# Kernel optimization log

Hardware: AMD Instinct MI355X
Metric: run time of the kernel (lower is better)

The kernel has to match this reference:

```python
import jax, jax.numpy as jnp
import numpy as np

B, N, M, D = 4, 4096, 4096, 128


def setup_inputs() -> dict:
    key = jax.random.key(0)
    kk, kq, kv = jax.random.split(key, 3)
    return {
        "k": jax.random.normal(kk, (B, N, D), dtype=jnp.float32),
        "q": jax.random.normal(kq, (B, M, D), dtype=jnp.float32),
        "v": jax.random.normal(kv, (B, M, D), dtype=jnp.float32),
    }


def reference(k, q, v):
    # scores: [B, N, M] = k @ q^T
    scores = jnp.einsum("bnd,bmd->bnm", k, q)
    # Original uses nn.Softmax() with no dim; torch's legacy rule resolves
    # dim=0 for 3-D inputs, so softmax is over the batch axis, applied twice.
    w = jax.nn.softmax(jax.nn.softmax(scores, axis=0), axis=0)
    out = jnp.einsum("bnm,bmd->bnd", w, v)
    return out
```

## Files before the change

### kernel.cpp

```cpp
#include <hip/hip_runtime.h>
#include <hip/hip_bf16.h>

#define NB 4
#define NN 4096
#define MM 4096
#define DD 128
#define BN 32
#define BM 64
#define NCH 4
#define OUT_ELEMS ((size_t)NB * NN * DD)

using f32x4  = __attribute__((ext_vector_type(4))) float;
using bf16x8 = __attribute__((ext_vector_type(8))) short;

__device__ __forceinline__ float fast_exp2(float x) {
  return __builtin_amdgcn_exp2f(x);
}

__device__ __forceinline__ int rfl(int x) {
  return __builtin_amdgcn_readfirstlane(x);
}

__device__ __forceinline__ short f2bf(float x) {
  union { __hip_bfloat16 h; short s; } u;
  u.h = __float2bfloat16(x);
  return u.s;
}

__device__ __forceinline__ bf16x8 pack8(const float* __restrict__ p) {
  float4 a = *(const float4*)p;
  float4 b = *(const float4*)(p + 4);
  bf16x8 r;
  r[0] = f2bf(a.x); r[1] = f2bf(a.y); r[2] = f2bf(a.z); r[3] = f2bf(a.w);
  r[4] = f2bf(b.x); r[5] = f2bf(b.y); r[6] = f2bf(b.z); r[7] = f2bf(b.w);
  return r;
}

__global__ __launch_bounds__(256) void zero_out_kernel(float4* __restrict__ out) {
  out[(size_t)blockIdx.x * 256 + threadIdx.x] = (float4){0.f, 0.f, 0.f, 0.f};
}

__global__ __launch_bounds__(256) void cvt_frag_kernel(const float* __restrict__ src,
                                                       unsigned short* __restrict__ dst) {
  const int blk = blockIdx.x;
  const int b = blk >> 8, rf = blk & 255;
  const int kf = threadIdx.x >> 6, l = threadIdx.x & 63;
  const int lr = l & 15, hg = l >> 4;
  const float* s = src + ((size_t)(b * 4096 + rf * 16 + lr) * DD + kf * 32 + hg * 8);
  bf16x8 r = pack8(s);
  *(bf16x8*)(dst + (((size_t)((b * 256 + rf) * 4 + kf)) << 9) + (l << 3)) = r;
}

__global__ __launch_bounds__(256) void transpose_v_frag_kernel(const float* __restrict__ v,
                                                               unsigned short* __restrict__ vt) {
  __shared__ unsigned short t[64][72];
  const int b = blockIdx.z, d0 = blockIdx.y * 64, m0 = blockIdx.x * 64;
  const int r = threadIdx.x >> 2, c4 = threadIdx.x & 3;
  const float* src = v + ((size_t)b * MM + m0 + r) * DD + d0 + c4 * 16;
  for (int j = 0; j < 4; ++j) {
    float4 x = *(const float4*)(src + j * 4);
    int dl = c4 * 16 + j * 4;
    t[dl + 0][r] = (unsigned short)f2bf(x.x);
    t[dl + 1][r] = (unsigned short)f2bf(x.y);
    t[dl + 2][r] = (unsigned short)f2bf(x.z);
    t[dl + 3][r] = (unsigned short)f2bf(x.w);
  }
  __syncthreads();
  const int s8 = threadIdx.x >> 5;
  const int dfl = s8 & 3, mtl = s8 >> 2;
  const int t32 = threadIdx.x & 31;
  for (int ll = 0; ll < 2; ++ll) {
    const int l = t32 * 2 + ll;
    const int lr = l & 15, hg = l >> 4;
    bf16x8 val = *(bf16x8*)&t[dfl * 16 + lr][mtl * 32 + hg * 8];
    *(bf16x8*)(vt + (((size_t)((b * 8 + (d0 >> 4) + dfl) * 128 + (m0 >> 5) + mtl)) << 9) +
               (l << 3)) = val;
  }
}

__global__ __launch_bounds__(256) void reduce4_frag_kernel(const float* __restrict__ p,
                                                           float* __restrict__ out) {
  const size_t idx = (size_t)blockIdx.x * 256 + threadIdx.x;
  f32x4 r = *(const f32x4*)(p + idx * 4);
  for (int c = 1; c < NCH; ++c) {
    f32x4 a = *(const f32x4*)(p + (size_t)c * OUT_ELEMS + idx * 4);
    r[0] += a[0]; r[1] += a[1]; r[2] += a[2]; r[3] += a[3];
  }
  const int l = (int)(idx & 63);
  const int djg = (int)((idx >> 6) & 7);
  const int nf = (int)((idx >> 9) & 255);
  const int bq = (int)(idx >> 17);
  const int lr = l & 15, hg = l >> 4;
  float* o = out + ((size_t)(bq * 4096 + nf * 16 + hg * 4) * DD + djg * 16 + lr);
  o[0] = r[0]; o[DD] = r[1]; o[2 * DD] = r[2]; o[3 * DD] = r[3];
}

#define LGKM0_SBAR()                                        \
  do {                                                      \
    asm volatile("s_waitcnt lgkmcnt(0)" ::: "memory");      \
    __builtin_amdgcn_sched_barrier(0);                      \
    __builtin_amdgcn_s_barrier();                           \
  } while (0)

template <bool WS, bool PART>
__global__ __launch_bounds__(512, 4) void attn_fused(
    const float* __restrict__ k, const float* __restrict__ q, const float* __restrict__ v,
    const unsigned short* __restrict__ kbt, const unsigned short* __restrict__ qbt,
    const unsigned short* __restrict__ vtt, float* __restrict__ outp) {
  __shared__ alignas(16) float s_pos[NB][8][64][4];
  __shared__ alignas(16) unsigned short Wl[NB][BN][BM];

  const int tid = threadIdx.x;
  const int wv = tid >> 6, l = tid & 63, lr = l & 15, hg = l >> 4;
  const int voff = l << 3;
  const int wg = blockIdx.x;
  const int cid = wg & (NCH - 1);
  const int n0 = (wg >> 2) * BN;
  const int it0 = cid * (MM / BM / NCH);
  const int it1 = it0 + (MM / BM / NCH);

  const int bq = wv >> 1, h = wv & 1;
  const int h_s = wv >> 2, fi_s = (wv >> 1) & 1, fj_s = wv & 1;

  bf16x8 ka[2][4];
  {
    const unsigned short* kp = WS ? (kbt + rfl(((bq * 256 + (n0 >> 4)) * 4) << 9)) : nullptr;
    for (int fi = 0; fi < 2; ++fi)
      for (int kf = 0; kf < 4; ++kf) {
        if (WS) ka[fi][kf] = *(const bf16x8*)(kp + fi * 2048 + kf * 512 + voff);
        else    ka[fi][kf] = pack8(k + ((size_t)bq * NN + n0 + fi * 16 + lr) * DD +
                                   kf * 32 + hg * 8);
      }
  }

  f32x4 acc[2][4];
  for (int fi = 0; fi < 2; ++fi)
    for (int dj = 0; dj < 4; ++dj) acc[fi][dj] = (f32x4){0.f, 0.f, 0.f, 0.f};

  bf16x8 vf[4][2];
  bf16x8 qf[2][4];

  auto load_q = [&](int it) {
    if (WS) {
      const unsigned short* qp = qbt + rfl(((bq * 256 + it * 4 + h * 2) * 4) << 9);
      for (int fj = 0; fj < 2; ++fj)
        for (int kf = 0; kf < 4; ++kf)
          qf[fj][kf] = *(const bf16x8*)(qp + fj * 2048 + kf * 512 + voff);
    } else {
      const int m0 = it * BM;
      for (int fj = 0; fj < 2; ++fj)
        for (int kf = 0; kf < 4; ++kf)
          qf[fj][kf] = pack8(q + ((size_t)bq * MM + m0 + h * 32 + fj * 16 + lr) * DD +
                             kf * 32 + hg * 8);
    }
  };

  auto qk_mfma = [&]() {
    f32x4 s[2][2];
    for (int fi = 0; fi < 2; ++fi)
      for (int fj = 0; fj < 2; ++fj) s[fi][fj] = (f32x4){0.f, 0.f, 0.f, 0.f};
    __builtin_amdgcn_s_setprio(1);
    for (int kf = 0; kf < 4; ++kf)
      for (int fi = 0; fi < 2; ++fi)
        for (int fj = 0; fj < 2; ++fj)
          s[fi][fj] = __builtin_amdgcn_mfma_f32_16x16x32_bf16(ka[fi][kf], qf[fj][kf],
                                                              s[fi][fj], 0, 0, 0);
    __builtin_amdgcn_s_setprio(0);
    for (int fi = 0; fi < 2; ++fi)
      for (int fj = 0; fj < 2; ++fj)
        *(f32x4*)&s_pos[bq][h * 4 + fi * 2 + fj][l][0] = s[fi][fj];
  };

  auto issue_v = [&](int it) {
    if (WS) {
      const unsigned short* vp = vtt + rfl((((bq * 8 + h * 4) * 128) + it * 2) << 9);
      for (int dj = 0; dj < 4; ++dj)
        for (int kf = 0; kf < 2; ++kf)
          vf[dj][kf] = *(const bf16x8*)(vp + dj * 65536 + kf * 512 + voff);
    } else {
      const int m0 = it * BM;
      for (int dj = 0; dj < 4; ++dj)
        for (int kf = 0; kf < 2; ++kf) {
          bf16x8 t;
          for (int e = 0; e < 8; ++e)
            t[e] = f2bf(v[((size_t)bq * MM + m0 + kf * 32 + hg * 8 + e) * DD +
                          h * 64 + dj * 16 + lr]);
          vf[dj][kf] = t;
        }
    }
  };

  auto do_sm = [&]() {
    f32x4 sv[NB];
    for (int bb = 0; bb < NB; ++bb) sv[bb] = *(f32x4*)&s_pos[bb][wv][l][0];
    const float L2E = 1.4426950408889634f;
    for (int qq = 0; qq < 4; ++qq) {
      float e0 = fast_exp2(sv[0][qq] * L2E), e1 = fast_exp2(sv[1][qq] * L2E);
      float e2 = fast_exp2(sv[2][qq] * L2E), e3 = fast_exp2(sv[3][qq] * L2E);
      float inv = __builtin_amdgcn_rcpf((e0 + e1) + (e2 + e3)) * L2E;
      float f0 = fast_exp2(e0 * inv), f1 = fast_exp2(e1 * inv);
      float f2v = fast_exp2(e2 * inv), f3 = fast_exp2(e3 * inv);
      float inv2 = __builtin_amdgcn_rcpf((f0 + f1) + (f2v + f3));
      const int n_loc = fi_s * 16 + hg * 4 + qq;
      const int m_loc = h_s * 32 + fj_s * 16 + lr;
      const int msw = m_loc ^ ((n_loc & 7) << 3);
      Wl[0][n_loc][msw] = (unsigned short)f2bf(f0 * inv2);
      Wl[1][n_loc][msw] = (unsigned short)f2bf(f1 * inv2);
      Wl[2][n_loc][msw] = (unsigned short)f2bf(f2v * inv2);
      Wl[3][n_loc][msw] = (unsigned short)f2bf(f3 * inv2);
    }
  };

  auto do_pv = [&]() {
    bf16x8 wf[2][2];
    for (int fi = 0; fi < 2; ++fi)
      for (int kf = 0; kf < 2; ++kf) {
        const int row = fi * 16 + lr, mo = kf * 32 + hg * 8;
        wf[fi][kf] = *(bf16x8*)&Wl[bq][row][mo ^ ((row & 7) << 3)];
      }
    __builtin_amdgcn_s_setprio(1);
    for (int kf = 0; kf < 2; ++kf)
      for (int fi = 0; fi < 2; ++fi)
        for (int dj = 0; dj < 4; ++dj)
          acc[fi][dj] = __builtin_amdgcn_mfma_f32_16x16x32_bf16(wf[fi][kf], vf[dj][kf],
                                                                acc[fi][dj], 0, 0, 0);
    __builtin_amdgcn_s_setprio(0);
  };

  load_q(it0);
  qk_mfma();
  LGKM0_SBAR();
  for (int t = it0; t < it1; ++t) {
    issue_v(t);
    do_sm();
    LGKM0_SBAR();
    do_pv();
    if (t + 1 < it1) {
      load_q(t + 1);
      qk_mfma();
    }
    LGKM0_SBAR();
  }

  if (PART) {
    float* dst = outp + (size_t)cid * OUT_ELEMS +
                 rfl((((bq * 256 + (n0 >> 4)) * 8 + h * 4)) << 8);
    for (int fi = 0; fi < 2; ++fi)
      for (int dj = 0; dj < 4; ++dj)
        *(f32x4*)(dst + fi * 2048 + dj * 256 + (l << 2)) = acc[fi][dj];
  } else {
    float* dst = outp;
    for (int fi = 0; fi < 2; ++fi)
      for (int dj = 0; dj < 4; ++dj)
        for (int qq = 0; qq < 4; ++qq)
          atomicAdd(dst + ((size_t)bq * NN + n0 + fi * 16 + hg * 4 + qq) * DD +
                        h * 64 + dj * 16 + lr,
                    acc[fi][dj][qq]);
  }
}

extern "C" void kernel_launch(void* const* d_in, const int* in_sizes, int n_in,
                              void* d_out, int out_size, void* d_ws, size_t ws_size,
                              hipStream_t stream) {
  (void)in_sizes; (void)n_in; (void)out_size;
  const float* k = (const float*)d_in[0];
  const float* q = (const float*)d_in[1];
  const float* v = (const float*)d_in[2];
  float* out = (float*)d_out;

  const size_t elems = (size_t)NB * MM * DD;
  const size_t need_bf = 3 * elems * sizeof(unsigned short);
  const size_t need_full = need_bf + NCH * OUT_ELEMS * sizeof(float);
  const bool use_ws = (d_ws != nullptr) && (ws_size >= need_bf);
  const bool use_part = (d_ws != nullptr) && (ws_size >= need_full);

  if (use_ws) {
    unsigned short* kbt = (unsigned short*)d_ws;
    unsigned short* qbt = kbt + elems;
    unsigned short* vtt = qbt + elems;
    cvt_frag_kernel<<<NB * 256, 256, 0, stream>>>(k, kbt);
    cvt_frag_kernel<<<NB * 256, 256, 0, stream>>>(q, qbt);
    transpose_v_frag_kernel<<<dim3(MM / 64, DD / 64, NB), 256, 0, stream>>>(v, vtt);
    if (use_part) {
      float* partials = (float*)((char*)d_ws + need_bf);
      attn_fused<true, true><<<dim3(NN / BN * NCH), 512, 0, stream>>>(k, q, v, kbt, qbt, vtt,
                                                                      partials);
      reduce4_frag_kernel<<<2048, 256, 0, stream>>>(partials, out);
    } else {
      zero_out_kernel<<<(NB * NN * DD) / 4 / 256, 256, 0, stream>>>((float4*)out);
      attn_fused<true, false><<<dim3(NN / BN * NCH), 512, 0, stream>>>(k, q, v, kbt, qbt, vtt,
                                                                       out);
    }
  } else {
    zero_out_kernel<<<(NB * NN * DD) / 4 / 256, 256, 0, stream>>>((float4*)out);
    attn_fused<false, false><<<dim3(NN / BN * NCH), 512, 0, stream>>>(k, q, v, nullptr,
                                                                      nullptr, nullptr, out);
  }
}
```

Before: 81.72 us.

## Transpose QK tile, store scores as bf16, and vectorize W writes to LDS

Swaps the MFMA operand order so each lane holds four consecutive m values for one n. The softmax weights can then be written to LDS as packed short4 stores instead of scalar 16-bit stores. Intermediate scores are staged in LDS as bf16 rather than fp32, halving that buffer and its traffic. The two K/Q conversion launches are merged into one 2-D grid. Rounding scores to bf16 before the double exp softmax adds precision error.

```diff
diff --git a/kernel.cpp b/kernel.cpp
--- a/kernel.cpp
+++ b/kernel.cpp
@@ -27,6 +27,12 @@
   return u.s;
 }
 
+__device__ __forceinline__ float bf2f(unsigned short s) {
+  union { float f; unsigned u; } u;
+  u.u = ((unsigned)s) << 16;
+  return u.f;
+}
+
 __device__ __forceinline__ bf16x8 pack8(const float* __restrict__ p) {
   float4 a = *(const float4*)p;
   float4 b = *(const float4*)(p + 4);
@@ -40,8 +46,12 @@
   out[(size_t)blockIdx.x * 256 + threadIdx.x] = (float4){0.f, 0.f, 0.f, 0.f};
 }
 
-__global__ __launch_bounds__(256) void cvt_frag_kernel(const float* __restrict__ src,
-                                                       unsigned short* __restrict__ dst) {
+__global__ __launch_bounds__(256) void cvt_frag_kernel(const float* __restrict__ s0,
+                                                       const float* __restrict__ s1,
+                                                       unsigned short* __restrict__ d0,
+                                                       unsigned short* __restrict__ d1) {
+  const float* src = blockIdx.y ? s1 : s0;
+  unsigned short* dst = blockIdx.y ? d1 : d0;
   const int blk = blockIdx.x;
   const int b = blk >> 8, rf = blk & 255;
   const int kf = threadIdx.x >> 6, l = threadIdx.x & 63;
@@ -107,7 +117,7 @@
     const float* __restrict__ k, const float* __restrict__ q, const float* __restrict__ v,
     const unsigned short* __restrict__ kbt, const unsigned short* __restrict__ qbt,
     const unsigned short* __restrict__ vtt, float* __restrict__ outp) {
-  __shared__ alignas(16) float s_pos[NB][8][64][4];
+  __shared__ alignas(8)  unsigned short s_pos[NB][8][64][4];
   __shared__ alignas(16) unsigned short Wl[NB][BN][BM];
 
   const int tid = threadIdx.x;
@@ -125,10 +135,10 @@
   bf16x8 ka[2][4];
   {
     const unsigned short* kp = WS ? (kbt + rfl(((bq * 256 + (n0 >> 4)) * 4) << 9)) : nullptr;
-    for (int fi = 0; fi < 2; ++fi)
+    for (int fn = 0; fn < 2; ++fn)
       for (int kf = 0; kf < 4; ++kf) {
-        if (WS) ka[fi][kf] = *(const bf16x8*)(kp + fi * 2048 + kf * 512 + voff);
-        else    ka[fi][kf] = pack8(k + ((size_t)bq * NN + n0 + fi * 16 + lr) * DD +
+        if (WS) ka[fn][kf] = *(const bf16x8*)(kp + fn * 2048 + kf * 512 + voff);
+        else    ka[fn][kf] = pack8(k + ((size_t)bq * NN + n0 + fn * 16 + lr) * DD +
                                    kf * 32 + hg * 8);
       }
   }
@@ -143,32 +153,36 @@
   auto load_q = [&](int it) {
     if (WS) {
       const unsigned short* qp = qbt + rfl(((bq * 256 + it * 4 + h * 2) * 4) << 9);
-      for (int fj = 0; fj < 2; ++fj)
+      for (int fm = 0; fm < 2; ++fm)
         for (int kf = 0; kf < 4; ++kf)
-          qf[fj][kf] = *(const bf16x8*)(qp + fj * 2048 + kf * 512 + voff);
+          qf[fm][kf] = *(const bf16x8*)(qp + fm * 2048 + kf * 512 + voff);
     } else {
       const int m0 = it * BM;
-      for (int fj = 0; fj < 2; ++fj)
+      for (int fm = 0; fm < 2; ++fm)
         for (int kf = 0; kf < 4; ++kf)
-          qf[fj][kf] = pack8(q + ((size_t)bq * MM + m0 + h * 32 + fj * 16 + lr) * DD +
+          qf[fm][kf] = pack8(q + ((size_t)bq * MM + m0 + h * 32 + fm * 16 + lr) * DD +
                              kf * 32 + hg * 8);
     }
   };
 
   auto qk_mfma = [&]() {
     f32x4 s[2][2];
-    for (int fi = 0; fi < 2; ++fi)
-      for (int fj = 0; fj < 2; ++fj) s[fi][fj] = (f32x4){0.f, 0.f, 0.f, 0.f};
+    for (int fm = 0; fm < 2; ++fm)
+      for (int fn = 0; fn < 2; ++fn) s[fm][fn] = (f32x4){0.f, 0.f, 0.f, 0.f};
     __builtin_amdgcn_s_setprio(1);
     for (int kf = 0; kf < 4; ++kf)
-      for (int fi = 0; fi < 2; ++fi)
-        for (int fj = 0; fj < 2; ++fj)
-          s[fi][fj] = __builtin_amdgcn_mfma_f32_16x16x32_bf16(ka[fi][kf], qf[fj][kf],
-                                                              s[fi][fj], 0, 0, 0);
+      for (int fm = 0; fm < 2; ++fm)
+        for (int fn = 0; fn < 2; ++fn)
+          s[fm][fn] = __builtin_amdgcn_mfma_f32_16x16x32_bf16(qf[fm][kf], ka[fn][kf],
+                                                              s[fm][fn], 0, 0, 0);
     __builtin_amdgcn_s_setprio(0);
-    for (int fi = 0; fi < 2; ++fi)
-      for (int fj = 0; fj < 2; ++fj)
-        *(f32x4*)&s_pos[bq][h * 4 + fi * 2 + fj][l][0] = s[fi][fj];
+    for (int fm = 0; fm < 2; ++fm)
+      for (int fn = 0; fn < 2; ++fn) {
+        short4 pk;
+        pk.x = f2bf(s[fm][fn][0]); pk.y = f2bf(s[fm][fn][1]);
+        pk.z = f2bf(s[fm][fn][2]); pk.w = f2bf(s[fm][fn][3]);
+        *(short4*)&s_pos[bq][h * 4 + fm * 2 + fn][l][0] = pk;
+      }
   };
 
   auto issue_v = [&](int it) {
@@ -191,8 +205,12 @@
   };
 
   auto do_sm = [&]() {
-    f32x4 sv[NB];
-    for (int bb = 0; bb < NB; ++bb) sv[bb] = *(f32x4*)&s_pos[bb][wv][l][0];
+    float sv[NB][4], w[NB][4];
+    for (int bb = 0; bb < NB; ++bb) {
+      short4 sp = *(short4*)&s_pos[bb][wv][l][0];
+      sv[bb][0] = bf2f((unsigned short)sp.x); sv[bb][1] = bf2f((unsigned short)sp.y);
+      sv[bb][2] = bf2f((unsigned short)sp.z); sv[bb][3] = bf2f((unsigned short)sp.w);
+    }
     const float L2E = 1.4426950408889634f;
     for (int qq = 0; qq < 4; ++qq) {
       float e0 = fast_exp2(sv[0][qq] * L2E), e1 = fast_exp2(sv[1][qq] * L2E);
@@ -201,13 +219,17 @@
       float f0 = fast_exp2(e0 * inv), f1 = fast_exp2(e1 * inv);
       float f2v = fast_exp2(e2 * inv), f3 = fast_exp2(e3 * inv);
       float inv2 = __builtin_amdgcn_rcpf((f0 + f1) + (f2v + f3));
-      const int n_loc = fi_s * 16 + hg * 4 + qq;
-      const int m_loc = h_s * 32 + fj_s * 16 + lr;
-      const int msw = m_loc ^ ((n_loc & 7) << 3);
-      Wl[0][n_loc][msw] = (unsigned short)f2bf(f0 * inv2);
-      Wl[1][n_loc][msw] = (unsigned short)f2bf(f1 * inv2);
-      Wl[2][n_loc][msw] = (unsigned short)f2bf(f2v * inv2);
-      Wl[3][n_loc][msw] = (unsigned short)f2bf(f3 * inv2);
+      w[0][qq] = f0 * inv2; w[1][qq] = f1 * inv2;
+      w[2][qq] = f2v * inv2; w[3][qq] = f3 * inv2;
+    }
+    const int n_loc = fj_s * 16 + lr;
+    const int mchunk = (h_s * 4 + fi_s * 2 + (hg >> 1)) ^ (n_loc & 7);
+    const int moff = mchunk * 8 + (hg & 1) * 4;
+    for (int bb = 0; bb < NB; ++bb) {
+      short4 pk;
+      pk.x = f2bf(w[bb][0]); pk.y = f2bf(w[bb][1]);
+      pk.z = f2bf(w[bb][2]); pk.w = f2bf(w[bb][3]);
+      *(short4*)&Wl[bb][n_loc][moff] = pk;
     }
   };
 
@@ -278,8 +300,7 @@
     unsigned short* kbt = (unsigned short*)d_ws;
     unsigned short* qbt = kbt + elems;
     unsigned short* vtt = qbt + elems;
-    cvt_frag_kernel<<<NB * 256, 256, 0, stream>>>(k, kbt);
-    cvt_frag_kernel<<<NB * 256, 256, 0, stream>>>(q, qbt);
+    cvt_frag_kernel<<<dim3(NB * 256, 2), 256, 0, stream>>>(k, q, kbt, qbt);
     transpose_v_frag_kernel<<<dim3(MM / 64, DD / 64, NB), 256, 0, stream>>>(v, vtt);
     if (use_part) {
       float* partials = (float*)((char*)d_ws + need_bf);
```

Result: faster. 79.27 us (-3.0%).
